# Kernel tuning notes

Measured on AMD Instinct MI355X. Metric: run time of the kernel, lower is better.

Reference implementation:

```python
import jax, jax.numpy as jnp
import numpy as np

N_NODES = 100000
DEGREE = 16
FEAT = 128
HID = 64
OUT = 16
BATCH = 4096
K = 12  # n_neibs


def setup_inputs() -> dict:
    key = jax.random.key(0)
    ks = jax.random.split(key, 12)
    idx0 = jax.random.randint(ks[0], (BATCH,), 0, N_NODES, dtype=jnp.int64 if jax.config.jax_enable_x64 else jnp.int32)
    buf1 = jax.random.randint(ks[1], (BATCH, K), 0, 1000000)
    buf2 = jax.random.randint(ks[2], (BATCH * K, K), 0, 1000000)
    indptr = jnp.arange(N_NODES) * DEGREE            # CSR row pointers (fixed degree)
    indices = jax.random.randint(ks[3], (N_NODES * DEGREE,), 0, N_NODES)
    degrees = jnp.full((N_NODES,), DEGREE, dtype=jnp.int32)
    emb_weight = jax.random.normal(ks[4], (N_NODES, FEAT), dtype=jnp.float32)
    enc_w = jax.random.normal(ks[5], (HID, FEAT), dtype=jnp.float32) * (1.0 / np.sqrt(FEAT))
    h1_w = jax.random.normal(ks[6], (HID, 2 * HID), dtype=jnp.float32) * (1.0 / np.sqrt(2 * HID))
    h1_b = jnp.zeros((HID,), jnp.float32)
    h2_w = jax.random.normal(ks[7], (HID, HID), dtype=jnp.float32) * (1.0 / np.sqrt(HID))
    h2_b = jnp.zeros((HID,), jnp.float32)
    out_w = jax.random.normal(ks[8], (OUT, HID), dtype=jnp.float32) * (1.0 / np.sqrt(HID))
    out_b = jnp.zeros((OUT,), jnp.float32)
    return dict(idx0=idx0, buf1=buf1, buf2=buf2, indptr=indptr, indices=indices,
                degrees=degrees, emb_weight=emb_weight, enc_w=enc_w,
                h1_w=h1_w, h1_b=h1_b, h2_w=h2_w, h2_b=h2_b, out_w=out_w, out_b=out_b)


def _sample_neighbors(nodes, buf, indptr, indices, degrees):
    # nodes: [M], buf: [M, K] random ints -> neighbor node ids [M, K]
    neibs = buf % degrees[nodes][:, None]
    offsets = indptr[nodes][:, None] + neibs
    return indices[offsets]


def reference(idx0, buf1, buf2, indptr, indices, degrees, emb_weight,
              enc_w, h1_w, h1_b, h2_w, h2_b, out_w, out_b):
    B = idx0.shape[0]
    idx1 = _sample_neighbors(idx0, buf1, indptr, indices, degrees)              # [B, K]
    idx2 = _sample_neighbors(idx1.reshape(B * K), buf2, indptr, indices, degrees)
    idx2 = idx2.reshape(B, K, K)                                                # [B, K, K]

    enc_1hop = jax.nn.relu(jnp.einsum('bkf,hf->bkh', emb_weight[idx1], enc_w))  # [B, K, H]
    enc_2hop = jax.nn.relu(jnp.einsum('bkjf,hf->bkjh', emb_weight[idx2], enc_w))
    avg_2hop = enc_2hop.mean(axis=-2)                                           # [B, K, H]

    h1 = jnp.concatenate([enc_1hop, avg_2hop], axis=-1)                         # [B, K, 2H]
    h1 = jax.nn.relu(jnp.einsum('bkc,hc->bkh', h1, h1_w) + h1_b)
    avg_1hop = h1.mean(axis=-2)                                                 # [B, H]
    h0 = jax.nn.relu(avg_1hop @ h2_w.T + h2_b)
    return h0 @ out_w.T + out_b                                                 # [B, OUT]
```

## Files before the change

### kernel.cpp

```cpp
#include <hip/hip_runtime.h>

#define NNODES 100000

typedef __attribute__((ext_vector_type(8))) short bf16x8;
typedef __attribute__((ext_vector_type(4))) float floatx4;

union PackU { uint4 u; bf16x8 v; };

__device__ __forceinline__ uint pack_hi2(float x0, float x1) {
    return (__float_as_uint(x1) & 0xFFFF0000u) | (__float_as_uint(x0) >> 16);
}
__device__ __forceinline__ uint pack_lo2(float x0, float x1) {
    float l0 = x0 - __uint_as_float(__float_as_uint(x0) & 0xFFFF0000u);
    float l1 = x1 - __uint_as_float(__float_as_uint(x1) & 0xFFFF0000u);
    return (__float_as_uint(l1) & 0xFFFF0000u) | (__float_as_uint(l0) >> 16);
}
__device__ __forceinline__ ushort bf_rne(float x) {
    unsigned u = __float_as_uint(x);
    return (ushort)((u + 0x7FFFu + ((u >> 16) & 1u)) >> 16);
}
__device__ __forceinline__ float lo16f(uint u) { return __uint_as_float(u << 16); }
__device__ __forceinline__ float hi16f(uint u) { return __uint_as_float(u & 0xFFFF0000u); }

__global__ __launch_bounds__(256) void k_prep(const float* __restrict__ enc_w,
                                              const float* __restrict__ h1_w,
                                              uint4* __restrict__ frgB,
                                              uint4* __restrict__ frgW) {
    const int t = threadIdx.x;
#pragma unroll
    for (int r = 0; r < 8; ++r) {
        int id = t + 256 * r;
        int lane = id & 63, m = lane & 15, q = lane >> 4;
        if (id < 1024) {
            int ks = (id >> 6) & 3, ht = id >> 8;
            const float* p = enc_w + (ht * 16 + m) * 128 + ks * 32 + q * 8;
            float4 f0 = *(const float4*)p, f1 = *(const float4*)(p + 4);
            frgB[((ht * 4 + ks) * 2 + 0) * 64 + lane] =
                (uint4){pack_hi2(f0.x, f0.y), pack_hi2(f0.z, f0.w),
                        pack_hi2(f1.x, f1.y), pack_hi2(f1.z, f1.w)};
            frgB[((ht * 4 + ks) * 2 + 1) * 64 + lane] =
                (uint4){pack_lo2(f0.x, f0.y), pack_lo2(f0.z, f0.w),
                        pack_lo2(f1.x, f1.y), pack_lo2(f1.z, f1.w)};
        } else {
            int id2 = id - 1024;
            int ks = (id2 >> 6) & 1, ot = id2 >> 7;
            int o2 = ot * 16 + m;
            const float* p = h1_w + (o2 & 63) * 128 + (o2 & 64) + ks * 32 + q * 8;
            float4 f0 = *(const float4*)p, f1 = *(const float4*)(p + 4);
            frgW[((ot * 2 + ks) * 2 + 0) * 64 + lane] =
                (uint4){pack_hi2(f0.x, f0.y), pack_hi2(f0.z, f0.w),
                        pack_hi2(f1.x, f1.y), pack_hi2(f1.z, f1.w)};
            frgW[((ot * 2 + ks) * 2 + 1) * 64 + lane] =
                (uint4){pack_lo2(f0.x, f0.y), pack_lo2(f0.z, f0.w),
                        pack_lo2(f1.x, f1.y), pack_lo2(f1.z, f1.w)};
        }
    }
}

__global__ __launch_bounds__(256) void k_gemm(const float* __restrict__ emb,
                                              const uint4* __restrict__ frgB,
                                              const uint4* __restrict__ frgW,
                                              ushort* __restrict__ encAB) {
    __shared__ ushort sE[2 * 64 * 72];
    const int t = threadIdx.x;
    const int n0 = blockIdx.x * 64;
    const int w = t >> 6, lane = t & 63;
    const int m = lane & 15, q = lane >> 4;

    int nn = n0 + w * 16 + m; if (nn > NNODES - 1) nn = NNODES - 1;
    const float* rowp = emb + (size_t)nn * 128 + q * 8;
    bf16x8 a_h[4], a_l[4];
#pragma unroll
    for (int ks = 0; ks < 4; ++ks) {
        float4 f0 = *(const float4*)(rowp + ks * 32);
        float4 f1 = *(const float4*)(rowp + ks * 32 + 4);
        PackU ph, pl;
        ph.u = (uint4){pack_hi2(f0.x, f0.y), pack_hi2(f0.z, f0.w),
                       pack_hi2(f1.x, f1.y), pack_hi2(f1.z, f1.w)};
        pl.u = (uint4){pack_lo2(f0.x, f0.y), pack_lo2(f0.z, f0.w),
                       pack_lo2(f1.x, f1.y), pack_lo2(f1.z, f1.w)};
        a_h[ks] = ph.v; a_l[ks] = pl.v;
    }

    const uint4* pB = frgB + lane;
    floatx4 acc[4] = {};
#pragma unroll
    for (int ht = 0; ht < 4; ++ht) {
#pragma unroll
        for (int ks = 0; ks < 4; ++ks) {
            PackU bh, bl;
            bh.u = pB[((ht * 4 + ks) * 2 + 0) * 64];
            bl.u = pB[((ht * 4 + ks) * 2 + 1) * 64];
            acc[ht] = __builtin_amdgcn_mfma_f32_16x16x32_bf16(a_h[ks], bh.v, acc[ht], 0, 0, 0);
            acc[ht] = __builtin_amdgcn_mfma_f32_16x16x32_bf16(a_l[ks], bh.v, acc[ht], 0, 0, 0);
            acc[ht] = __builtin_amdgcn_mfma_f32_16x16x32_bf16(a_h[ks], bl.v, acc[ht], 0, 0, 0);
        }
    }

#pragma unroll
    for (int ht = 0; ht < 4; ++ht)
#pragma unroll
        for (int i = 0; i < 4; ++i) {
            float v = fmaxf(acc[ht][i], 0.f);
            int row = w * 16 + q * 4 + i, col = ht * 16 + m;
            uint uv = __float_as_uint(v);
            sE[row * 72 + col] = (ushort)(uv >> 16);
            float lo = v - __uint_as_float(uv & 0xFFFF0000u);
            sE[64 * 72 + row * 72 + col] = (ushort)(__float_as_uint(lo) >> 16);
        }

    bf16x8 e_h[2], e_l[2];
    {
        const ushort* pE = sE + (w * 16 + m) * 72 + q * 8;
#pragma unroll
        for (int ks = 0; ks < 2; ++ks) {
            e_h[ks] = *(const bf16x8*)(pE + ks * 32);
            e_l[ks] = *(const bf16x8*)(pE + 64 * 72 + ks * 32);
        }
    }
    const uint4* pW = frgW + lane;
    floatx4 acc2[8] = {};
#pragma unroll
    for (int ot = 0; ot < 8; ++ot) {
#pragma unroll
        for (int ks = 0; ks < 2; ++ks) {
            PackU wh, wl;
            wh.u = pW[((ot * 2 + ks) * 2 + 0) * 64];
            wl.u = pW[((ot * 2 + ks) * 2 + 1) * 64];
            acc2[ot] = __builtin_amdgcn_mfma_f32_16x16x32_bf16(e_h[ks], wh.v, acc2[ot], 0, 0, 0);
            acc2[ot] = __builtin_amdgcn_mfma_f32_16x16x32_bf16(e_l[ks], wh.v, acc2[ot], 0, 0, 0);
            acc2[ot] = __builtin_amdgcn_mfma_f32_16x16x32_bf16(e_h[ks], wl.v, acc2[ot], 0, 0, 0);
        }
    }
#pragma unroll
    for (int ot = 0; ot < 8; ++ot)
#pragma unroll
        for (int i = 0; i < 4; ++i) {
            int n = n0 + w * 16 + q * 4 + i;
            if (n < NNODES) encAB[n * 128 + ot * 16 + m] = bf_rne(acc2[ot][i]);
        }
}

__global__ __launch_bounds__(256) void k_gather_head(const int* __restrict__ idx0,
                                                     const int* __restrict__ buf1,
                                                     const int* __restrict__ buf2,
                                                     const int* __restrict__ indices,
                                                     const ushort* __restrict__ encAB,
                                                     const float* __restrict__ h1_b,
                                                     const float* __restrict__ h2_w,
                                                     const float* __restrict__ h2_b,
                                                     const float* __restrict__ out_w,
                                                     const float* __restrict__ out_b,
                                                     float* __restrict__ out) {
    __shared__ int s_idx1[48];
    __shared__ int s_idx2[576];
    __shared__ float sW2[64 * 65];
    __shared__ float sWo[64 * 17];
    __shared__ float sAvg[4][64];
    __shared__ float sH0[4][64];

    const int t = threadIdx.x;
    const int b0 = blockIdx.x * 4;

    if (t < 48) {
        int bl = t / 12;
        s_idx1[t] = indices[idx0[b0 + bl] * 16 + (buf1[b0 * 12 + t] & 15)];
    }
#pragma unroll
    for (int r = 0; r < 16; ++r) {
        int e = t + 256 * r;
        sW2[(e & 63) * 65 + (e >> 6)] = h2_w[e];
    }
#pragma unroll
    for (int r = 0; r < 4; ++r) {
        int e = t + 256 * r;
        sWo[(e & 63) * 17 + (e >> 6)] = out_w[e];
    }
    __syncthreads();

#pragma unroll
    for (int r = 0; r < 3; ++r) {
        int s = t + 256 * r;
        if (s < 576) {
            int bk = s / 12;
            s_idx2[s] = indices[s_idx1[bk] * 16 + (buf2[b0 * 144 + s] & 15)];
        }
    }
    __syncthreads();

    const int w = t >> 6, lane = t & 63;
    const int pp = lane >> 5, c = lane & 31;
    const uint* __restrict__ encAB32 = (const uint*)encAB;
    const int* myi1 = &s_idx1[w * 12];
    const int* myi2 = &s_idx2[w * 144];
    float2 bb = *(const float2*)&h1_b[2 * c];
    float hs0 = 0.f, hs1 = 0.f;
#pragma unroll 3
    for (int k = 0; k < 12; ++k) {
        uint av = encAB32[myi1[k] * 64 + c];
        float s0 = 0.f, s1 = 0.f;
#pragma unroll
        for (int jj = 0; jj < 6; ++jj) {
            uint v = encAB32[myi2[k * 12 + 2 * jj + pp] * 64 + 32 + c];
            s0 += lo16f(v); s1 += hi16f(v);
        }
        s0 += __shfl_xor(s0, 32);
        s1 += __shfl_xor(s1, 32);
        hs0 += fmaxf(lo16f(av) + s0 * (1.f / 12.f) + bb.x, 0.f);
        hs1 += fmaxf(hi16f(av) + s1 * (1.f / 12.f) + bb.y, 0.f);
    }
    if (pp == 0) {
        sAvg[w][2 * c]     = hs0 * (1.f / 12.f);
        sAvg[w][2 * c + 1] = hs1 * (1.f / 12.f);
    }
    __syncthreads();

    {
        float acc = h2_b[lane];
#pragma unroll 8
        for (int i = 0; i < 64; ++i)
            acc += sAvg[w][i] * sW2[i * 65 + lane];
        sH0[w][lane] = fmaxf(acc, 0.f);
    }
    __syncthreads();
    if (t < 64) {
        int g2 = t >> 4, o = t & 15;
        float acc2 = out_b[o];
#pragma unroll 8
        for (int i = 0; i < 64; ++i)
            acc2 += sH0[g2][i] * sWo[i * 17 + o];
        out[(b0 + g2) * 16 + o] = acc2;
    }
}

extern "C" void kernel_launch(void* const* d_in, const int* in_sizes, int n_in,
                              void* d_out, int out_size, void* d_ws, size_t ws_size,
                              hipStream_t stream) {
    const int*   idx0    = (const int*)d_in[0];
    const int*   buf1    = (const int*)d_in[1];
    const int*   buf2    = (const int*)d_in[2];
    const int*   indices = (const int*)d_in[4];
    const float* emb     = (const float*)d_in[6];
    const float* enc_w   = (const float*)d_in[7];
    const float* h1_w    = (const float*)d_in[8];
    const float* h1_b    = (const float*)d_in[9];
    const float* h2_w    = (const float*)d_in[10];
    const float* h2_b    = (const float*)d_in[11];
    const float* out_w   = (const float*)d_in[12];
    const float* out_b   = (const float*)d_in[13];
    (void)d_in[3]; (void)d_in[5];
    float* out = (float*)d_out;

    ushort* encAB = (ushort*)d_ws;
    uint4* frgB = (uint4*)((char*)d_ws + 25600000);
    uint4* frgW = frgB + 2048;

    k_prep<<<1, 256, 0, stream>>>(enc_w, h1_w, frgB, frgW);
    k_gemm<<<1563, 256, 0, stream>>>(emb, frgB, frgW, encAB);
    k_gather_head<<<1024, 256, 0, stream>>>(idx0, buf1, buf2, indices, encAB,
                                            h1_b, h2_w, h2_b, out_w, out_b, out);
}
```

Measured before the change: 158.8 us.

## Process 64-node tile per single wavefront to reuse weight fragments across rows

The node-encoding GEMM kernel now uses one 64-lane wavefront per 64-node block instead of four wavefronts. Each lane loops over four 16-row sub-tiles, so each loaded enc_w and h1_w fragment is reused across all four instead of being loaded by every wave. The aim is to cut redundant weight-fragment loads and block overhead. In exchange, the block count stays at 1563 with only 64 threads each, which lowers per-block parallelism, raises register pressure (16 accumulators) and serialises more MFMA work per wave. That may reduce latency hiding for the streaming embedding reads.

```diff
diff --git a/kernel.cpp b/kernel.cpp
--- a/kernel.cpp
+++ b/kernel.cpp
@@ -57,88 +57,91 @@
     }
 }
 
-__global__ __launch_bounds__(256) void k_gemm(const float* __restrict__ emb,
-                                              const uint4* __restrict__ frgB,
-                                              const uint4* __restrict__ frgW,
-                                              ushort* __restrict__ encAB) {
+__global__ __launch_bounds__(64) void k_gemm(const float* __restrict__ emb,
+                                             const uint4* __restrict__ frgB,
+                                             const uint4* __restrict__ frgW,
+                                             ushort* __restrict__ encAB) {
     __shared__ ushort sE[2 * 64 * 72];
-    const int t = threadIdx.x;
+    const int lane = threadIdx.x;
     const int n0 = blockIdx.x * 64;
-    const int w = t >> 6, lane = t & 63;
     const int m = lane & 15, q = lane >> 4;
 
-    int nn = n0 + w * 16 + m; if (nn > NNODES - 1) nn = NNODES - 1;
-    const float* rowp = emb + (size_t)nn * 128 + q * 8;
-    bf16x8 a_h[4], a_l[4];
+    const uint4* pB = frgB + lane;
+
+    floatx4 acc[4][4] = {};
 #pragma unroll
     for (int ks = 0; ks < 4; ++ks) {
-        float4 f0 = *(const float4*)(rowp + ks * 32);
-        float4 f1 = *(const float4*)(rowp + ks * 32 + 4);
-        PackU ph, pl;
-        ph.u = (uint4){pack_hi2(f0.x, f0.y), pack_hi2(f0.z, f0.w),
-                       pack_hi2(f1.x, f1.y), pack_hi2(f1.z, f1.w)};
-        pl.u = (uint4){pack_lo2(f0.x, f0.y), pack_lo2(f0.z, f0.w),
-                       pack_lo2(f1.x, f1.y), pack_lo2(f1.z, f1.w)};
-        a_h[ks] = ph.v; a_l[ks] = pl.v;
-    }
-
-    const uint4* pB = frgB + lane;
-    floatx4 acc[4] = {};
-#pragma unroll
-    for (int ht = 0; ht < 4; ++ht) {
-#pragma unroll
-        for (int ks = 0; ks < 4; ++ks) {
+        bf16x8 a_h[4], a_l[4];
+#pragma unroll
+        for (int s = 0; s < 4; ++s) {
+            int nn = n0 + s * 16 + m; if (nn > NNODES - 1) nn = NNODES - 1;
+            const float* rowp = emb + (size_t)nn * 128 + ks * 32 + q * 8;
+            float4 f0 = *(const float4*)rowp;
+            float4 f1 = *(const float4*)(rowp + 4);
+            PackU ph, pl;
+            ph.u = (uint4){pack_hi2(f0.x, f0.y), pack_hi2(f0.z, f0.w),
+                           pack_hi2(f1.x, f1.y), pack_hi2(f1.z, f1.w)};
+            pl.u = (uint4){pack_lo2(f0.x, f0.y), pack_lo2(f0.z, f0.w),
+                           pack_lo2(f1.x, f1.y), pack_lo2(f1.z, f1.w)};
+            a_h[s] = ph.v; a_l[s] = pl.v;
+        }
+#pragma unroll
+        for (int ht = 0; ht < 4; ++ht) {
             PackU bh, bl;
             bh.u = pB[((ht * 4 + ks) * 2 + 0) * 64];
             bl.u = pB[((ht * 4 + ks) * 2 + 1) * 64];
-            acc[ht] = __builtin_amdgcn_mfma_f32_16x16x32_bf16(a_h[ks], bh.v, acc[ht], 0, 0, 0);
-            acc[ht] = __builtin_amdgcn_mfma_f32_16x16x32_bf16(a_l[ks], bh.v, acc[ht], 0, 0, 0);
-            acc[ht] = __builtin_amdgcn_mfma_f32_16x16x32_bf16(a_h[ks], bl.v, acc[ht], 0, 0, 0);
-        }
-    }
-
-#pragma unroll
-    for (int ht = 0; ht < 4; ++ht)
-#pragma unroll
-        for (int i = 0; i < 4; ++i) {
-            float v = fmaxf(acc[ht][i], 0.f);
-            int row = w * 16 + q * 4 + i, col = ht * 16 + m;
-            uint uv = __float_as_uint(v);
-            sE[row * 72 + col] = (ushort)(uv >> 16);
-            float lo = v - __uint_as_float(uv & 0xFFFF0000u);
-            sE[64 * 72 + row * 72 + col] = (ushort)(__float_as_uint(lo) >> 16);
-        }
-
-    bf16x8 e_h[2], e_l[2];
-    {
-        const ushort* pE = sE + (w * 16 + m) * 72 + q * 8;
-#pragma unroll
-        for (int ks = 0; ks < 2; ++ks) {
-            e_h[ks] = *(const bf16x8*)(pE + ks * 32);
-            e_l[ks] = *(const bf16x8*)(pE + 64 * 72 + ks * 32);
-        }
-    }
+#pragma unroll
+            for (int s = 0; s < 4; ++s) {
+                acc[s][ht] = __builtin_amdgcn_mfma_f32_16x16x32_bf16(a_h[s], bh.v, acc[s][ht], 0, 0, 0);
+                acc[s][ht] = __builtin_amdgcn_mfma_f32_16x16x32_bf16(a_l[s], bh.v, acc[s][ht], 0, 0, 0);
+                acc[s][ht] = __builtin_amdgcn_mfma_f32_16x16x32_bf16(a_h[s], bl.v, acc[s][ht], 0, 0, 0);
+            }
+        }
+    }
+
+#pragma unroll
+    for (int s = 0; s < 4; ++s)
+#pragma unroll
+        for (int ht = 0; ht < 4; ++ht)
+#pragma unroll
+            for (int i = 0; i < 4; ++i) {
+                float v = fmaxf(acc[s][ht][i], 0.f);
+                int row = s * 16 + q * 4 + i, col = ht * 16 + m;
+                uint uv = __float_as_uint(v);
+                sE[row * 72 + col] = (ushort)(uv >> 16);
+                float lo = v - __uint_as_float(uv & 0xFFFF0000u);
+                sE[64 * 72 + row * 72 + col] = (ushort)(__float_as_uint(lo) >> 16);
+            }
+
     const uint4* pW = frgW + lane;
-    floatx4 acc2[8] = {};
 #pragma unroll
     for (int ot = 0; ot < 8; ++ot) {
-#pragma unroll
-        for (int ks = 0; ks < 2; ++ks) {
-            PackU wh, wl;
-            wh.u = pW[((ot * 2 + ks) * 2 + 0) * 64];
-            wl.u = pW[((ot * 2 + ks) * 2 + 1) * 64];
-            acc2[ot] = __builtin_amdgcn_mfma_f32_16x16x32_bf16(e_h[ks], wh.v, acc2[ot], 0, 0, 0);
-            acc2[ot] = __builtin_amdgcn_mfma_f32_16x16x32_bf16(e_l[ks], wh.v, acc2[ot], 0, 0, 0);
-            acc2[ot] = __builtin_amdgcn_mfma_f32_16x16x32_bf16(e_h[ks], wl.v, acc2[ot], 0, 0, 0);
-        }
-    }
-#pragma unroll
-    for (int ot = 0; ot < 8; ++ot)
-#pragma unroll
-        for (int i = 0; i < 4; ++i) {
-            int n = n0 + w * 16 + q * 4 + i;
-            if (n < NNODES) encAB[n * 128 + ot * 16 + m] = bf_rne(acc2[ot][i]);
-        }
+        PackU wh0, wl0, wh1, wl1;
+        wh0.u = pW[((ot * 2 + 0) * 2 + 0) * 64];
+        wl0.u = pW[((ot * 2 + 0) * 2 + 1) * 64];
+        wh1.u = pW[((ot * 2 + 1) * 2 + 0) * 64];
+        wl1.u = pW[((ot * 2 + 1) * 2 + 1) * 64];
+#pragma unroll
+        for (int c = 0; c < 4; ++c) {
+            const ushort* pE = sE + (c * 16 + m) * 72 + q * 8;
+            bf16x8 e_h0 = *(const bf16x8*)(pE);
+            bf16x8 e_h1 = *(const bf16x8*)(pE + 32);
+            bf16x8 e_l0 = *(const bf16x8*)(pE + 64 * 72);
+            bf16x8 e_l1 = *(const bf16x8*)(pE + 64 * 72 + 32);
+            floatx4 acc2 = {};
+            acc2 = __builtin_amdgcn_mfma_f32_16x16x32_bf16(e_h0, wh0.v, acc2, 0, 0, 0);
+            acc2 = __builtin_amdgcn_mfma_f32_16x16x32_bf16(e_l0, wh0.v, acc2, 0, 0, 0);
+            acc2 = __builtin_amdgcn_mfma_f32_16x16x32_bf16(e_h0, wl0.v, acc2, 0, 0, 0);
+            acc2 = __builtin_amdgcn_mfma_f32_16x16x32_bf16(e_h1, wh1.v, acc2, 0, 0, 0);
+            acc2 = __builtin_amdgcn_mfma_f32_16x16x32_bf16(e_l1, wh1.v, acc2, 0, 0, 0);
+            acc2 = __builtin_amdgcn_mfma_f32_16x16x32_bf16(e_h1, wl1.v, acc2, 0, 0, 0);
+#pragma unroll
+            for (int i = 0; i < 4; ++i) {
+                int n = n0 + c * 16 + q * 4 + i;
+                if (n < NNODES) encAB[n * 128 + ot * 16 + m] = bf_rne(acc2[i]);
+            }
+        }
+    }
 }
 
 __global__ __launch_bounds__(256) void k_gather_head(const int* __restrict__ idx0,
@@ -256,7 +259,7 @@
     uint4* frgW = frgB + 2048;
 
     k_prep<<<1, 256, 0, stream>>>(enc_w, h1_w, frgB, frgW);
-    k_gemm<<<1563, 256, 0, stream>>>(emb, frgB, frgW, encAB);
+    k_gemm<<<1563, 64, 0, stream>>>(emb, frgB, frgW, encAB);
     k_gather_head<<<1024, 256, 0, stream>>>(idx0, buf1, buf2, indices, encAB,
                                             h1_b, h2_w, h2_b, out_w, out_b, out);
 }
```

New measurement: 149.8 us. 1.06x faster.
